# Optimization experiments

Measured on AMD Instinct MI355X. Metric: run time of the kernel, lower is better.

## Reference

```python
import jax, jax.numpy as jnp
import numpy as np

A0, A1, A2 = 1.0, 1.0, 0.5  # Taylor coefficients of exp around 0 (p=2)

B, H, N, D = 2, 16, 4096, 32


def setup_inputs() -> dict:
    key = jax.random.key(0)
    kq, kk, kv = jax.random.split(key, 3)
    q = jax.random.normal(kq, (B, H, N, D), dtype=jnp.float32)
    k = jax.random.normal(kk, (B, H, N, D), dtype=jnp.float32)
    v = jax.random.normal(kv, (B, H, N, D), dtype=jnp.float32)
    return {"q": q, "k": k, "v": v}


def reference(q, k, v):
    # fastmax_function with p=2, mask=False, normalize=False, dropout=0 -> temperature=1
    b, h, n, d = q.shape
    # quadratic feature maps: flatten of outer products, [b,h,n,d*d]
    q2 = (q[..., :, None] * q[..., None, :]).reshape(b, h, n, d * d)
    k2 = (k[..., :, None] * k[..., None, :]).reshape(b, h, n, d * d)
    # numerator: a0*sum(v) + a1*q(k^T v) + a2*q2(k2^T v)
    second_term = A1 * jnp.einsum('bhnd,bhne->bhde', k, v)           # [b,h,d,d]
    third_term = A2 * jnp.einsum('bhnf,bhne->bhfe', k2, v)           # [b,h,d^2,d]
    ans = (jnp.einsum('bhnd,bhde->bhne', q, second_term)
           + jnp.einsum('bhnf,bhfe->bhne', q2, third_term)
           + A0 * jnp.sum(v, axis=-2, keepdims=True))                 # [b,h,n,d]
    # denominator: a0*n + a1*q.sum(k) + a2*q2.sum(k2)
    div = (A0 * n
           + A1 * jnp.einsum('bhnd,bhd->bhn', q, jnp.sum(k, axis=-2))
           + A2 * jnp.einsum('bhnf,bhf->bhn', q2, jnp.sum(k2, axis=-2)))  # [b,h,n]
    return ans / div[..., None]
```

## Files before the change

### kernel.cpp

```cpp
#include <hip/hip_runtime.h>

#define NTOK 4096
#define NBH  32
#define NF   1088
#define NE   33
#define GTF_BH 52224

typedef _Float16 half_t;
typedef _Float16 half8 __attribute__((ext_vector_type(8)));
typedef _Float16 half4v __attribute__((ext_vector_type(4)));
typedef float f32x4 __attribute__((ext_vector_type(4)));
typedef unsigned int u32;

#define MFMA16(A,B,C) __builtin_amdgcn_mfma_f32_16x16x32_f16((A),(B),(C),0,0,0)

#define ASYNC_CP16(dst_lds, src_glb) \
    __builtin_amdgcn_global_load_lds( \
        (const __attribute__((address_space(1))) u32*)(const void*)(src_glb), \
        (__attribute__((address_space(3))) u32*)(void*)(dst_lds), 16, 0, 0)

static __device__ __forceinline__ half8 splat8(half_t x) {
    return (half8){x, x, x, x, x, x, x, x};
}

__global__ __launch_bounds__(256)
void t_kernel(const float* __restrict__ kin, const float* __restrict__ vin,
              half_t* __restrict__ kTg, half_t* __restrict__ vTg)
{
    const int nb = blockIdx.x;
    const int bh = blockIdx.y;
    const int t  = threadIdx.x;
    __shared__ __align__(16) half_t tile[32 * 272];
    const size_t inbase = ((size_t)bh * NTOK + nb * 256) * 32;

    for (int pass = 0; pass < 2; ++pass) {
        const float* src = pass ? vin : kin;
        half_t* dstg     = pass ? vTg : kTg;
        if (pass) __syncthreads();
        const float4* s4 = (const float4*)(src + inbase);
        #pragma unroll
        for (int r = 0; r < 8; ++r) {
            int f4 = t + 256 * r;
            int n = f4 >> 3, d4 = f4 & 7;
            float4 vv = s4[f4];
            int nn = n ^ ((d4 & 7) << 3);
            int d0 = d4 * 4;
            tile[(d0 + 0) * 272 + nn] = (half_t)vv.x;
            tile[(d0 + 1) * 272 + nn] = (half_t)vv.y;
            tile[(d0 + 2) * 272 + nn] = (half_t)vv.z;
            tile[(d0 + 3) * 272 + nn] = (half_t)vv.w;
        }
        __syncthreads();
        #pragma unroll
        for (int cc = 0; cc < 4; ++cc) {
            int lin = t + 256 * cc;
            int d = lin >> 5, ch = lin & 31;
            int sw = (d >> 2) & 7;
            half8 val = *(const half8*)&tile[d * 272 + ((ch ^ sw) << 3)];
            *(half8*)&dstg[((size_t)bh * 32 + d) * NTOK + nb * 256 + ch * 8] = val;
        }
    }
}

__global__ __launch_bounds__(256)
void a_kernel(const half_t* __restrict__ kTg, const half_t* __restrict__ vTg,
              half_t* __restrict__ P, int Kc)
{
    const int x  = blockIdx.x;
    const int bh = x & (NBH - 1);
    const int kc = x >> 5;
    const int mb = blockIdx.y;
    const int t = threadIdx.x;
    const int w = t >> 6, lane = t & 63, l16 = lane & 15, quad = lane >> 4;

    __shared__ __align__(16) half_t kT[32 * 128];
    __shared__ __align__(16) half_t vT[32 * 128];

    const int pw = mb * 256 + w * 64;
    const bool active = (pw < NF);
    const int mode = (mb == 0 && w == 0) ? 1 : ((mb == 4) ? 2 : 0);
    const int i0 = (pw >= 32 && pw < NF) ? ((pw - 32) >> 5) : 0;
    const half8 h05 = splat8((half_t)0.5f);

    f32x4 acc[3][4];
    #pragma unroll
    for (int a = 0; a < 3; ++a)
        #pragma unroll
        for (int b = 0; b < 4; ++b)
            acc[a][b] = (f32x4){0.f, 0.f, 0.f, 0.f};

    const size_t gbase = (size_t)bh * 32 * NTOK;
    const int nPer = NTOK / Kc;
    const int nStages = nPer >> 7;

    const int c0 = t,        r0 = c0 >> 4, p0s = (c0 & 15) ^ (r0 & 15);
    const int c1 = 256 + t,  r1 = c1 >> 4, p1s = (c1 & 15) ^ (r1 & 15);

    for (int st = 0; st < nStages; ++st) {
        __syncthreads();
        const int nbase = kc * nPer + st * 128;
        {
            const half_t* gk0 = kTg + gbase + (size_t)r0 * NTOK + nbase + p0s * 8;
            const half_t* gk1 = kTg + gbase + (size_t)r1 * NTOK + nbase + p1s * 8;
            const half_t* gv0 = vTg + gbase + (size_t)r0 * NTOK + nbase + p0s * 8;
            const half_t* gv1 = vTg + gbase + (size_t)r1 * NTOK + nbase + p1s * 8;
            ASYNC_CP16(kT + (size_t)w * 512,        gk0);
            ASYNC_CP16(kT + 2048 + (size_t)w * 512, gk1);
            ASYNC_CP16(vT + (size_t)w * 512,        gv0);
            ASYNC_CP16(vT + 2048 + (size_t)w * 512, gv1);
        }
        __syncthreads();
        if (!active) continue;
        #pragma unroll
        for (int kk = 0; kk < 4; ++kk) {
            const int c = kk * 4 + quad;
            const int offL = l16 * 128 + ((c ^ l16) << 3);
            const int offH = (l16 + 16) * 128 + ((c ^ l16) << 3);
            half8 bf0 = *(const half8*)&vT[offL];
            half8 bf1 = *(const half8*)&vT[offH];
            half_t onec = (l16 == 0) ? (half_t)1 : (half_t)0;
            half8 bf2 = {onec, onec, onec, onec, onec, onec, onec, onec};
            half8 kj0 = *(const half8*)&kT[offL];
            half8 kj1 = *(const half8*)&kT[offH];
            half8 af[4];
            bool skip3 = false;
            if (mode == 1) {
                half8 ki = *(const half8*)&kT[(c ^ 0) << 3];
                ki = ki * h05;
                af[0] = kj0; af[1] = kj1;
                af[2] = ki * kj0; af[3] = ki * kj1;
            } else if (mode == 2) {
                half8 ki = *(const half8*)&kT[31 * 128 + ((c ^ 15) << 3)];
                ki = ki * h05;
                af[0] = ki * kj0; af[1] = ki * kj1;
                af[2] = bf2;
                af[3] = bf2;
                skip3 = true;
            } else {
                half8 kia = *(const half8*)&kT[i0 * 128 + ((c ^ (i0 & 15)) << 3)];
                half8 kib = *(const half8*)&kT[(i0 + 1) * 128 + ((c ^ ((i0 + 1) & 15)) << 3)];
                kia = kia * h05;
                kib = kib * h05;
                af[0] = kia * kj0; af[1] = kia * kj1;
                af[2] = kib * kj0; af[3] = kib * kj1;
            }
            #pragma unroll
            for (int mt = 0; mt < 4; ++mt) {
                if (skip3 && mt == 3) continue;
                acc[0][mt] = MFMA16(af[mt], bf0, acc[0][mt]);
                acc[1][mt] = MFMA16(af[mt], bf1, acc[1][mt]);
                acc[2][mt] = MFMA16(af[mt], bf2, acc[2][mt]);
            }
        }
    }
    if (active) {
        half_t* Pb = P + ((size_t)kc * NBH + bh) * NE * NF;
        #pragma unroll
        for (int mt = 0; mt < 4; ++mt) {
            int p0 = pw + mt * 16 + quad * 4;
            half4v h0 = {(half_t)acc[0][mt][0], (half_t)acc[0][mt][1],
                         (half_t)acc[0][mt][2], (half_t)acc[0][mt][3]};
            half4v h1 = {(half_t)acc[1][mt][0], (half_t)acc[1][mt][1],
                         (half_t)acc[1][mt][2], (half_t)acc[1][mt][3]};
            *(half4v*)&Pb[(size_t)l16 * NF + p0] = h0;
            *(half4v*)&Pb[(size_t)(l16 + 16) * NF + p0] = h1;
            if (l16 == 0) {
                half4v h2 = {(half_t)acc[2][mt][0], (half_t)acc[2][mt][1],
                             (half_t)acc[2][mt][2], (half_t)acc[2][mt][3]};
                *(half4v*)&Pb[(size_t)32 * NF + p0] = h2;
            }
        }
    }
}

__global__ __launch_bounds__(256)
void ar_kernel(const half_t* __restrict__ P, half_t* __restrict__ GtF, int Kc)
{
    const int NP8 = NBH * NE * NF / 8;
    const int idx = blockIdx.x * 256 + threadIdx.x;
    if (idx >= NP8) return;
    float s[8] = {0.f, 0.f, 0.f, 0.f, 0.f, 0.f, 0.f, 0.f};
    for (int c = 0; c < Kc; ++c) {
        half8 h = *(const half8*)&P[(size_t)c * (NBH * NE * NF) + (size_t)idx * 8];
        #pragma unroll
        for (int j = 0; j < 8; ++j) s[j] += (float)h[j];
    }
    half8 o;
    #pragma unroll
    for (int j = 0; j < 8; ++j) o[j] = (half_t)s[j];
    int row = idx / 136;
    int p8 = idx - row * 136;
    int e = row % 33, bhh = row / 33;
    int kt = p8 >> 2, quad = p8 & 3;
    int rr = e >> 4, l16 = e & 15;
    size_t dst8 = (size_t)bhh * (GTF_BH / 8)
                + (size_t)(kt * 3 + rr) * 64 + quad * 16 + l16;
    *(half8*)&GtF[dst8 * 8] = o;
}

__global__ __launch_bounds__(256)
void b_kernel(const float* __restrict__ qin, const half_t* __restrict__ GtF,
              float* __restrict__ out)
{
    const int bh = blockIdx.x, mbq = blockIdx.y;
    const int t = threadIdx.x, w = t >> 6, lane = t & 63;
    const int l16 = lane & 15, quad = lane >> 4;
    __shared__ __align__(16) half_t qs[256 * 40];
    __shared__ __align__(16) half_t qsP[32 * 272];
    __shared__ float denl[256];
    const size_t nbase = (size_t)bh * NTOK + mbq * 256;

    const float4* q4 = (const float4*)(qin + nbase * 32);
    #pragma unroll
    for (int r = 0; r < 8; ++r) {
        int f4 = t + 256 * r, n = f4 >> 3, d4 = f4 & 7;
        float4 vv = q4[f4];
        half4v h = {(half_t)vv.x, (half_t)vv.y, (half_t)vv.z, (half_t)vv.w};
        *(half4v*)&qs[n * 40 + d4 * 4] = h;
        int pb = (n >> 6) * 64 + (n & 15) * 4 + ((n >> 4) & 3);
        qsP[(4 * d4 + 0) * 272 + pb] = h[0];
        qsP[(4 * d4 + 1) * 272 + pb] = h[1];
        qsP[(4 * d4 + 2) * 272 + pb] = h[2];
        qsP[(4 * d4 + 3) * 272 + pb] = h[3];
    }
    __syncthreads();

    const int rbase = w * 64;
    half8 vq[4];
    #pragma unroll
    for (int mt = 0; mt < 4; ++mt)
        vq[mt] = *(const half8*)&qs[(rbase + mt * 16 + l16) * 40 + quad * 8];

    f32x4 acc[3][4];
    #pragma unroll
    for (int a = 0; a < 3; ++a)
        #pragma unroll
        for (int b = 0; b < 4; ++b)
            acc[a][b] = (f32x4){0.f, 0.f, 0.f, 0.f};

    const half_t* Gb = GtF + (size_t)bh * GTF_BH + (size_t)lane * 8;
    const int sOff = w * 64 + l16 * 4;

#define LDF(kt, B) do { \
    _Pragma("unroll") \
    for (int rr = 0; rr < 3; ++rr) \
        (B)[rr] = *(const half8*)&Gb[(size_t)(((kt) * 3 + rr) * 64) * 8]; \
} while (0)

    half8 B0[3], B1[3], B2[3], B3[3];
    LDF(0, B0); LDF(1, B1); LDF(2, B2);

    {
        LDF(3, B3);
        #pragma unroll
        for (int mt = 0; mt < 4; ++mt) {
            acc[0][mt] = MFMA16(vq[mt], B0[0], acc[0][mt]);
            acc[1][mt] = MFMA16(vq[mt], B0[1], acc[1][mt]);
            acc[2][mt] = MFMA16(vq[mt], B0[2], acc[2][mt]);
        }
        #pragma unroll
        for (int rr = 0; rr < 3; ++rr) { B0[rr] = B1[rr]; B1[rr] = B2[rr]; B2[rr] = B3[rr]; }
    }
    #pragma unroll 1
    for (int kt = 1; kt <= 32; ++kt) {
        const int ktp = (kt + 3 <= 33) ? kt + 3 : 33;
        LDF(ktp, B3);
        half4v sv = *(const half4v*)&qsP[(kt - 1) * 272 + sOff];
        half8 af[4];
        #pragma unroll
        for (int mt = 0; mt < 4; ++mt)
            af[mt] = vq[mt] * splat8(sv[mt]);
        #pragma unroll
        for (int mt = 0; mt < 4; ++mt) {
            acc[0][mt] = MFMA16(af[mt], B0[0], acc[0][mt]);
            acc[1][mt] = MFMA16(af[mt], B0[1], acc[1][mt]);
            acc[2][mt] = MFMA16(af[mt], B0[2], acc[2][mt]);
        }
        #pragma unroll
        for (int rr = 0; rr < 3; ++rr) { B0[rr] = B1[rr]; B1[rr] = B2[rr]; B2[rr] = B3[rr]; }
    }
    {
        half8 cf = {};
        if (quad == 0) cf[0] = (half_t)1;
        #pragma unroll
        for (int mt = 0; mt < 4; ++mt) {
            acc[0][mt] = MFMA16(cf, B0[0], acc[0][mt]);
            acc[1][mt] = MFMA16(cf, B0[1], acc[1][mt]);
            acc[2][mt] = MFMA16(cf, B0[2], acc[2][mt]);
        }
    }
#undef LDF

    if (l16 == 0) {
        #pragma unroll
        for (int mt = 0; mt < 4; ++mt)
            #pragma unroll
            for (int r = 0; r < 4; ++r)
                denl[rbase + mt * 16 + quad * 4 + r] = acc[2][mt][r];
    }
    __syncthreads();
    #pragma unroll
    for (int mt = 0; mt < 4; ++mt) {
        float inv[4];
        #pragma unroll
        for (int r = 0; r < 4; ++r)
            inv[r] = __builtin_amdgcn_rcpf(denl[rbase + mt * 16 + quad * 4 + r]);
        #pragma unroll
        for (int r = 0; r < 4; ++r) {
            size_t ro = (nbase + rbase + mt * 16 + quad * 4 + r) * 32;
            out[ro + l16] = acc[0][mt][r] * inv[r];
            out[ro + l16 + 16] = acc[1][mt][r] * inv[r];
        }
    }
}

extern "C" void kernel_launch(void* const* d_in, const int* in_sizes, int n_in,
                              void* d_out, int out_size, void* d_ws, size_t ws_size,
                              hipStream_t stream)
{
    const float* q = (const float*)d_in[0];
    const float* k = (const float*)d_in[1];
    const float* v = (const float*)d_in[2];
    float* out = (float*)d_out;

    const size_t planeBytes = (size_t)NBH * NE * NF * 2;
    const size_t ktBytes = (size_t)NBH * 32 * NTOK * 2;
    const size_t gtBytes = (size_t)NBH * GTF_BH * 2;
    int Kc = 8;
    while (Kc > 1 && ((size_t)Kc * planeBytes + 2 * ktBytes + gtBytes) > ws_size)
        Kc >>= 1;

    half_t* P = (half_t*)d_ws;
    half_t* kTg = (half_t*)((char*)d_ws + (size_t)Kc * planeBytes);
    half_t* vTg = kTg + (size_t)NBH * 32 * NTOK;
    half_t* GtF = vTg + (size_t)NBH * 32 * NTOK;

    t_kernel<<<dim3(16, NBH), 256, 0, stream>>>(k, v, kTg, vTg);
    a_kernel<<<dim3(Kc * NBH, 5), 256, 0, stream>>>(kTg, vTg, P, Kc);
    ar_kernel<<<561, 256, 0, stream>>>(P, GtF, Kc);
    b_kernel<<<dim3(NBH, 16), 256, 0, stream>>>(q, GtF, out);
}
```

Measured before the change: 142.3 us.

## Double-buffer K/V tiles in a_kernel and rebalance feature rows over two blocks

```diff
diff --git a/kernel.cpp b/kernel.cpp
--- a/kernel.cpp
+++ b/kernel.cpp
@@ -62,114 +62,118 @@
     }
 }
 
-__global__ __launch_bounds__(256)
+template<int NMT>
+__device__ __forceinline__ void a_body(
+    const half_t* __restrict__ kTg, const half_t* __restrict__ vTg,
+    half_t* __restrict__ P, int Kc, int bh, int kc, int pw,
+    int t, int w, int l16, int quad, half_t* kT0, half_t* vT0)
+{
+    const half8 h05 = splat8((half_t)0.5f);
+    f32x4 acc[NMT][3];
+    #pragma unroll
+    for (int m = 0; m < NMT; ++m)
+        #pragma unroll
+        for (int e = 0; e < 3; ++e)
+            acc[m][e] = (f32x4){0.f, 0.f, 0.f, 0.f};
+
+    const size_t gbase = (size_t)bh * 32 * NTOK;
+    const int nPer = NTOK / Kc;
+    const int nStages = nPer >> 7;
+
+    const int c0 = t,        r0 = c0 >> 4, p0s = (c0 & 15) ^ (r0 & 15);
+    const int c1 = 256 + t,  r1 = c1 >> 4, p1s = (c1 & 15) ^ (r1 & 15);
+
+    auto issue = [&](int buf, int nbase) {
+        const half_t* gk0 = kTg + gbase + (size_t)r0 * NTOK + nbase + p0s * 8;
+        const half_t* gk1 = kTg + gbase + (size_t)r1 * NTOK + nbase + p1s * 8;
+        const half_t* gv0 = vTg + gbase + (size_t)r0 * NTOK + nbase + p0s * 8;
+        const half_t* gv1 = vTg + gbase + (size_t)r1 * NTOK + nbase + p1s * 8;
+        half_t* kb = kT0 + buf * 4096;
+        half_t* vb = vT0 + buf * 4096;
+        ASYNC_CP16(kb + (size_t)w * 512,        gk0);
+        ASYNC_CP16(kb + 2048 + (size_t)w * 512, gk1);
+        ASYNC_CP16(vb + (size_t)w * 512,        gv0);
+        ASYNC_CP16(vb + 2048 + (size_t)w * 512, gv1);
+    };
+
+    issue(0, kc * nPer);
+
+    for (int st = 0; st < nStages; ++st) {
+        const int cur = st & 1;
+        __syncthreads();
+        if (st + 1 < nStages) issue(cur ^ 1, kc * nPer + (st + 1) * 128);
+        const half_t* kb = kT0 + cur * 4096;
+        const half_t* vb = vT0 + cur * 4096;
+        #pragma unroll
+        for (int kk = 0; kk < 4; ++kk) {
+            const int c = kk * 4 + quad;
+            const int shL = ((c ^ l16) << 3);
+            half8 kj0 = *(const half8*)&kb[l16 * 128 + shL];
+            half8 kj1 = *(const half8*)&kb[(l16 + 16) * 128 + shL];
+            half8 bf0 = *(const half8*)&vb[l16 * 128 + shL];
+            half8 bf1 = *(const half8*)&vb[(l16 + 16) * 128 + shL];
+            half_t onec = (l16 == 0) ? (half_t)1 : (half_t)0;
+            half8 bf2 = {onec, onec, onec, onec, onec, onec, onec, onec};
+            #pragma unroll
+            for (int mt = 0; mt < NMT; ++mt) {
+                const int pm = pw + mt * 16;
+                half8 af;
+                if (pm < 32) {
+                    af = pm ? kj1 : kj0;
+                } else if (pm == 1056) {
+                    af = bf2;
+                } else if (pm > 1056) {
+                    continue;
+                } else {
+                    const int i = (pm - 32) >> 5;
+                    const int j0 = (pm - 32) & 31;
+                    half8 ki = *(const half8*)&kb[i * 128 + ((c ^ (i & 15)) << 3)];
+                    ki = ki * h05;
+                    af = ki * (j0 ? kj1 : kj0);
+                }
+                acc[mt][0] = MFMA16(af, bf0, acc[mt][0]);
+                acc[mt][1] = MFMA16(af, bf1, acc[mt][1]);
+                acc[mt][2] = MFMA16(af, bf2, acc[mt][2]);
+            }
+        }
+    }
+
+    half_t* Pb = P + ((size_t)kc * NBH + bh) * NE * NF;
+    #pragma unroll
+    for (int mt = 0; mt < NMT; ++mt) {
+        int p0 = pw + mt * 16 + quad * 4;
+        half4v h0 = {(half_t)acc[mt][0][0], (half_t)acc[mt][0][1],
+                     (half_t)acc[mt][0][2], (half_t)acc[mt][0][3]};
+        half4v h1 = {(half_t)acc[mt][1][0], (half_t)acc[mt][1][1],
+                     (half_t)acc[mt][1][2], (half_t)acc[mt][1][3]};
+        *(half4v*)&Pb[(size_t)l16 * NF + p0] = h0;
+        *(half4v*)&Pb[(size_t)(l16 + 16) * NF + p0] = h1;
+        if (l16 == 0) {
+            half4v h2 = {(half_t)acc[mt][2][0], (half_t)acc[mt][2][1],
+                         (half_t)acc[mt][2][2], (half_t)acc[mt][2][3]};
+            *(half4v*)&Pb[(size_t)32 * NF + p0] = h2;
+        }
+    }
+}
+
+__global__ __launch_bounds__(256, 2)
 void a_kernel(const half_t* __restrict__ kTg, const half_t* __restrict__ vTg,
               half_t* __restrict__ P, int Kc)
 {
     const int x  = blockIdx.x;
     const int bh = x & (NBH - 1);
     const int kc = x >> 5;
-    const int mb = blockIdx.y;
+    const int half = blockIdx.y;
     const int t = threadIdx.x;
     const int w = t >> 6, lane = t & 63, l16 = lane & 15, quad = lane >> 4;
 
-    __shared__ __align__(16) half_t kT[32 * 128];
-    __shared__ __align__(16) half_t vT[32 * 128];
-
-    const int pw = mb * 256 + w * 64;
-    const bool active = (pw < NF);
-    const int mode = (mb == 0 && w == 0) ? 1 : ((mb == 4) ? 2 : 0);
-    const int i0 = (pw >= 32 && pw < NF) ? ((pw - 32) >> 5) : 0;
-    const half8 h05 = splat8((half_t)0.5f);
-
-    f32x4 acc[3][4];
-    #pragma unroll
-    for (int a = 0; a < 3; ++a)
-        #pragma unroll
-        for (int b = 0; b < 4; ++b)
-            acc[a][b] = (f32x4){0.f, 0.f, 0.f, 0.f};
-
-    const size_t gbase = (size_t)bh * 32 * NTOK;
-    const int nPer = NTOK / Kc;
-    const int nStages = nPer >> 7;
-
-    const int c0 = t,        r0 = c0 >> 4, p0s = (c0 & 15) ^ (r0 & 15);
-    const int c1 = 256 + t,  r1 = c1 >> 4, p1s = (c1 & 15) ^ (r1 & 15);
-
-    for (int st = 0; st < nStages; ++st) {
-        __syncthreads();
-        const int nbase = kc * nPer + st * 128;
-        {
-            const half_t* gk0 = kTg + gbase + (size_t)r0 * NTOK + nbase + p0s * 8;
-            const half_t* gk1 = kTg + gbase + (size_t)r1 * NTOK + nbase + p1s * 8;
-            const half_t* gv0 = vTg + gbase + (size_t)r0 * NTOK + nbase + p0s * 8;
-            const half_t* gv1 = vTg + gbase + (size_t)r1 * NTOK + nbase + p1s * 8;
-            ASYNC_CP16(kT + (size_t)w * 512,        gk0);
-            ASYNC_CP16(kT + 2048 + (size_t)w * 512, gk1);
-            ASYNC_CP16(vT + (size_t)w * 512,        gv0);
-            ASYNC_CP16(vT + 2048 + (size_t)w * 512, gv1);
-        }
-        __syncthreads();
-        if (!active) continue;
-        #pragma unroll
-        for (int kk = 0; kk < 4; ++kk) {
-            const int c = kk * 4 + quad;
-            const int offL = l16 * 128 + ((c ^ l16) << 3);
-            const int offH = (l16 + 16) * 128 + ((c ^ l16) << 3);
-            half8 bf0 = *(const half8*)&vT[offL];
-            half8 bf1 = *(const half8*)&vT[offH];
-            half_t onec = (l16 == 0) ? (half_t)1 : (half_t)0;
-            half8 bf2 = {onec, onec, onec, onec, onec, onec, onec, onec};
-            half8 kj0 = *(const half8*)&kT[offL];
-            half8 kj1 = *(const half8*)&kT[offH];
-            half8 af[4];
-            bool skip3 = false;
-            if (mode == 1) {
-                half8 ki = *(const half8*)&kT[(c ^ 0) << 3];
-                ki = ki * h05;
-                af[0] = kj0; af[1] = kj1;
-                af[2] = ki * kj0; af[3] = ki * kj1;
-            } else if (mode == 2) {
-                half8 ki = *(const half8*)&kT[31 * 128 + ((c ^ 15) << 3)];
-                ki = ki * h05;
-                af[0] = ki * kj0; af[1] = ki * kj1;
-                af[2] = bf2;
-                af[3] = bf2;
-                skip3 = true;
-            } else {
-                half8 kia = *(const half8*)&kT[i0 * 128 + ((c ^ (i0 & 15)) << 3)];
-                half8 kib = *(const half8*)&kT[(i0 + 1) * 128 + ((c ^ ((i0 + 1) & 15)) << 3)];
-                kia = kia * h05;
-                kib = kib * h05;
-                af[0] = kia * kj0; af[1] = kia * kj1;
-                af[2] = kib * kj0; af[3] = kib * kj1;
-            }
-            #pragma unroll
-            for (int mt = 0; mt < 4; ++mt) {
-                if (skip3 && mt == 3) continue;
-                acc[0][mt] = MFMA16(af[mt], bf0, acc[0][mt]);
-                acc[1][mt] = MFMA16(af[mt], bf1, acc[1][mt]);
-                acc[2][mt] = MFMA16(af[mt], bf2, acc[2][mt]);
-            }
-        }
-    }
-    if (active) {
-        half_t* Pb = P + ((size_t)kc * NBH + bh) * NE * NF;
-        #pragma unroll
-        for (int mt = 0; mt < 4; ++mt) {
-            int p0 = pw + mt * 16 + quad * 4;
-            half4v h0 = {(half_t)acc[0][mt][0], (half_t)acc[0][mt][1],
-                         (half_t)acc[0][mt][2], (half_t)acc[0][mt][3]};
-            half4v h1 = {(half_t)acc[1][mt][0], (half_t)acc[1][mt][1],
-                         (half_t)acc[1][mt][2], (half_t)acc[1][mt][3]};
-            *(half4v*)&Pb[(size_t)l16 * NF + p0] = h0;
-            *(half4v*)&Pb[(size_t)(l16 + 16) * NF + p0] = h1;
-            if (l16 == 0) {
-                half4v h2 = {(half_t)acc[2][mt][0], (half_t)acc[2][mt][1],
-                             (half_t)acc[2][mt][2], (half_t)acc[2][mt][3]};
-                *(half4v*)&Pb[(size_t)32 * NF + p0] = h2;
-            }
-        }
+    __shared__ __align__(16) half_t kT[2 * 4096];
+    __shared__ __align__(16) half_t vT[2 * 4096];
+
+    if (half == 0) {
+        a_body<9>(kTg, vTg, P, Kc, bh, kc, w * 144, t, w, l16, quad, kT, vT);
+    } else {
+        a_body<8>(kTg, vTg, P, Kc, bh, kc, 576 + w * 128, t, w, l16, quad, kT, vT);
     }
 }
 
@@ -336,7 +340,7 @@
     half_t* GtF = vTg + (size_t)NBH * 32 * NTOK;
 
     t_kernel<<<dim3(16, NBH), 256, 0, stream>>>(k, v, kTg, vTg);
-    a_kernel<<<dim3(Kc * NBH, 5), 256, 0, stream>>>(kTg, vTg, P, Kc);
+    a_kernel<<<dim3(Kc * NBH, 2), 256, 0, stream>>>(kTg, vTg, P, Kc);
     ar_kernel<<<561, 256, 0, stream>>>(P, GtF, Kc);
     b_kernel<<<dim3(NBH, 16), 256, 0, stream>>>(q, GtF, out);
 }
```

New measurement: 137.9 us. 3.1% less time.
